# Performance work log

Measured on AMD Instinct MI355X. Metric: run time of the kernel, lower is better.

The kernel has to match this reference:

```python
import jax, jax.numpy as jnp
import numpy as np

B, S, D = 4, 2048, 512
H, DK, DV = 8, 64, 64


def setup_inputs() -> dict:
    key = jax.random.key(0)
    ks = jax.random.split(key, 9)
    inp = {
        "input_Q": jax.random.normal(ks[0], (B, S, D), dtype=jnp.float32),
        "input_K": jax.random.normal(ks[1], (B, S, D), dtype=jnp.float32),
        "input_V": jax.random.normal(ks[2], (B, S, D), dtype=jnp.float32),
        "attn_mask": jax.random.bernoulli(ks[3], 0.1, (B, S, S)),
        "other": jax.random.normal(ks[4], (B, S, S), dtype=jnp.float32),
        # nn.Linear weights stored [out_features, in_features]
        "W_Q": jax.random.normal(ks[5], (H * DK, D), dtype=jnp.float32) * (1.0 / np.sqrt(D)),
        "W_K": jax.random.normal(ks[6], (H * DK, D), dtype=jnp.float32) * (1.0 / np.sqrt(D)),
        "W_V": jax.random.normal(ks[7], (H * DV, D), dtype=jnp.float32) * (1.0 / np.sqrt(D)),
        "W_fc": jax.random.normal(ks[8], (D, H * DV), dtype=jnp.float32) * (1.0 / np.sqrt(H * DV)),
    }
    return inp


def reference(input_Q, input_K, input_V, attn_mask, other, W_Q, W_K, W_V, W_fc):
    b, s, _ = input_Q.shape
    # projections: y = x @ W.T, then split heads -> [B,H,S,dk]
    Q = (input_Q @ W_Q.T).reshape(b, s, H, DK).transpose(0, 2, 1, 3)
    K = (input_K @ W_K.T).reshape(b, s, H, DK).transpose(0, 2, 1, 3)
    V = (input_V @ W_V.T).reshape(b, s, H, DV).transpose(0, 2, 1, 3)
    scale = 1.0 / np.sqrt(DK).astype(np.float32)
    scores = jnp.einsum("bhqd,bhkd->bhqk", Q, K) * scale  # [B,H,S,S]
    scores = scores + other[:, None, :, :]  # additive bias broadcast over heads
    scores = jnp.where(attn_mask[:, None, :, :], jnp.float32(-1e9), scores)
    attn = jax.nn.softmax(scores, axis=-1)
    context = jnp.einsum("bhqk,bhkd->bhqd", attn, V)  # [B,H,S,DV]
    context = context.transpose(0, 2, 1, 3).reshape(b, s, H * DV)
    output = context @ W_fc.T  # dropout is identity at inference
    return (output, attn)
```

## Files before the change

### kernel.cpp

```cpp
#include <hip/hip_runtime.h>

#define BB 4
#define SS 2048
#define DDIM 512
#define HH 8
#define MTOK (BB*SS)
#define BHN (BB*HH)

typedef _Float16 f16;
typedef __attribute__((ext_vector_type(8))) _Float16 half8;
typedef __attribute__((ext_vector_type(4))) _Float16 half4;
typedef __attribute__((ext_vector_type(4))) float float4v;
typedef __attribute__((ext_vector_type(4))) int int4v;

#define SCALE_L2E 0.180336880073616f
#define L2E 1.44269504088896f
#define EBIAS 4.0f
#define MASKVAL -65504.0f

__device__ __forceinline__ float4v mfma_k32(half8 a, half8 b, float4v c) {
  return __builtin_amdgcn_mfma_f32_16x16x32_f16(a, b, c, 0, 0, 0);
}

__device__ __forceinline__ half8 cvt8(float4v a, float4v b) {
  half8 r;
  r[0] = (f16)a[0]; r[1] = (f16)a[1]; r[2] = (f16)a[2]; r[3] = (f16)a[3];
  r[4] = (f16)b[0]; r[5] = (f16)b[1]; r[6] = (f16)b[2]; r[7] = (f16)b[3];
  return r;
}

__global__ __launch_bounds__(256) void detect_mask_kernel(
    const unsigned int* __restrict__ m, unsigned int* __restrict__ flag) {
  unsigned int v = 0;
  const int base = blockIdx.x * 1024;
  for (int j = threadIdx.x; j < 1024; j += 256)
    if (m[base + j] > 1u) v = 1u;
  if (v) atomicOr(flag, 1u);
}

__global__ __launch_bounds__(256) void gemm_qkv(
    const float* __restrict__ inQ, const float* __restrict__ inK,
    const float* __restrict__ inV, const float* __restrict__ WQ,
    const float* __restrict__ WK, const float* __restrict__ WV,
    f16* __restrict__ Qp, f16* __restrict__ Kfrag, f16* __restrict__ Vfrag) {
  __shared__ f16 As[128][40];
  __shared__ f16 Bs[128][40];
  const int z = blockIdx.z;
  const float* A = (z == 0) ? inQ : (z == 1) ? inK : inV;
  const float* W = (z == 0) ? WQ : (z == 1) ? WK : WV;
  const int t = threadIdx.x;
  const int bm = blockIdx.x * 128;
  const int bn = blockIdx.y * 128;
  const int w = t >> 6, ln = t & 63;
  const int wr = w >> 1, wc = w & 1;
  const int lr = ln & 15, lg = ln >> 4;
  const int srow = t >> 1, scol = (t & 1) * 16;

  float4v acc[4][4] = {};

  for (int k0 = 0; k0 < 512; k0 += 32) {
    {
      const float* ap = A + (size_t)(bm + srow) * 512 + k0 + scol;
      float4v x0 = *(const float4v*)ap,       x1 = *(const float4v*)(ap + 4);
      float4v x2 = *(const float4v*)(ap + 8), x3 = *(const float4v*)(ap + 12);
      *(half8*)&As[srow][scol]     = cvt8(x0, x1);
      *(half8*)&As[srow][scol + 8] = cvt8(x2, x3);
    }
    {
      const float* wp = W + (size_t)(bn + srow) * 512 + k0 + scol;
      float4v x0 = *(const float4v*)wp,       x1 = *(const float4v*)(wp + 4);
      float4v x2 = *(const float4v*)(wp + 8), x3 = *(const float4v*)(wp + 12);
      *(half8*)&Bs[srow][scol]     = cvt8(x0, x1);
      *(half8*)&Bs[srow][scol + 8] = cvt8(x2, x3);
    }
    __syncthreads();
    half8 af[4], bf[4];
    #pragma unroll
    for (int m = 0; m < 4; m++) af[m] = *(const half8*)&As[wr * 64 + m * 16 + lr][lg * 8];
    #pragma unroll
    for (int n = 0; n < 4; n++) bf[n] = *(const half8*)&Bs[wc * 64 + n * 16 + lr][lg * 8];
    #pragma unroll
    for (int m = 0; m < 4; m++)
      #pragma unroll
      for (int n = 0; n < 4; n++) acc[m][n] = mfma_k32(af[m], bf[n], acc[m][n]);
    __syncthreads();
  }

  #pragma unroll
  for (int m = 0; m < 4; m++) {
    int row = bm + wr * 64 + m * 16 + lg * 4;
    #pragma unroll
    for (int n = 0; n < 4; n++) {
      int col = bn + wc * 64 + n * 16 + lr;
      int b_ = row >> 11, s_ = row & 2047, h_ = col >> 6, d_ = col & 63;
      if (z == 0) {
        #pragma unroll
        for (int r = 0; r < 4; r++)
          Qp[(size_t)(row + r) * 512 + col] = (f16)acc[m][n][r];
      } else if (z == 1) {
        #pragma unroll
        for (int r = 0; r < 4; r++) {
          int tok = s_ + r;
          Kfrag[((((size_t)(b_ * 8 + h_)) * 128 + (tok >> 4)) * 2 + (d_ >> 5)) * 512 +
                ((tok & 15) + 16 * ((d_ >> 3) & 3)) * 8 + (d_ & 7)] =
              (f16)acc[m][n][r];
        }
      } else {
        half4 ph;
        ph[0] = (f16)acc[m][n][0]; ph[1] = (f16)acc[m][n][1];
        ph[2] = (f16)acc[m][n][2]; ph[3] = (f16)acc[m][n][3];
        *(half4*)&Vfrag[((((size_t)(b_ * 8 + h_)) * 64 + (s_ >> 5)) * 4 + (d_ >> 4)) * 512 +
                        ((d_ & 15) + 16 * ((s_ >> 2) & 3)) * 8 + ((s_ >> 2) & 4)] = ph;
      }
    }
  }
}

__global__ __launch_bounds__(256) void gemm_out(const f16* __restrict__ ctx,
                                                const float* __restrict__ W,
                                                float* __restrict__ Out) {
  __shared__ f16 As[128][40];
  __shared__ f16 Bs[128][40];
  const int t = threadIdx.x;
  const int bm = blockIdx.x * 128;
  const int bn = blockIdx.y * 128;
  const int w = t >> 6, ln = t & 63;
  const int wr = w >> 1, wc = w & 1;
  const int lr = ln & 15, lg = ln >> 4;
  const int srow = t >> 1, scol = (t & 1) * 16;

  float4v acc[4][4] = {};

  for (int k0 = 0; k0 < 512; k0 += 32) {
    {
      const f16* ap = ctx + (size_t)(bm + srow) * 512 + k0 + scol;
      *(half8*)&As[srow][scol]     = *(const half8*)(ap);
      *(half8*)&As[srow][scol + 8] = *(const half8*)(ap + 8);
    }
    {
      const float* wp = W + (size_t)(bn + srow) * 512 + k0 + scol;
      float4v x0 = *(const float4v*)wp,       x1 = *(const float4v*)(wp + 4);
      float4v x2 = *(const float4v*)(wp + 8), x3 = *(const float4v*)(wp + 12);
      *(half8*)&Bs[srow][scol]     = cvt8(x0, x1);
      *(half8*)&Bs[srow][scol + 8] = cvt8(x2, x3);
    }
    __syncthreads();
    half8 af[4], bf[4];
    #pragma unroll
    for (int m = 0; m < 4; m++) af[m] = *(const half8*)&As[wr * 64 + m * 16 + lr][lg * 8];
    #pragma unroll
    for (int n = 0; n < 4; n++) bf[n] = *(const half8*)&Bs[wc * 64 + n * 16 + lr][lg * 8];
    #pragma unroll
    for (int m = 0; m < 4; m++)
      #pragma unroll
      for (int n = 0; n < 4; n++) acc[m][n] = mfma_k32(af[m], bf[n], acc[m][n]);
    __syncthreads();
  }

  #pragma unroll
  for (int m = 0; m < 4; m++) {
    int row = bm + wr * 64 + m * 16 + lg * 4;
    #pragma unroll
    for (int n = 0; n < 4; n++) {
      int col = bn + wc * 64 + n * 16 + lr;
      #pragma unroll
      for (int r = 0; r < 4; r++)
        Out[(size_t)(row + r) * 512 + col] = acc[m][n][r];
    }
  }
}

#define LOADT(dst, base, st) {                                  \
    const f16* p_ = (base) + (size_t)(st) * 2048;               \
    dst##0 = *(const half8*)(p_);                               \
    dst##1 = *(const half8*)(p_ + 512);                         \
    dst##2 = *(const half8*)(p_ + 1024);                        \
    dst##3 = *(const half8*)(p_ + 1536); }

__global__ __launch_bounds__(1024) void attn_fused(
    const f16* __restrict__ Qp, const f16* __restrict__ Kfrag,
    const f16* __restrict__ Vfrag, const float* __restrict__ other,
    const unsigned char* __restrict__ mask8, const int* __restrict__ mask32,
    const unsigned int* __restrict__ flag, float* __restrict__ attn_out,
    f16* __restrict__ ctx) {
  __shared__ f16 othm[16][2056];
  __shared__ float red[16][16];
  __shared__ float red2[16][16][66];

  const int t = threadIdx.x;
  const int bid = blockIdx.x;
  const int b = bid & 3;
  const int qblk = (bid >> 2) * 16;
  const int w = t >> 6, ln = t & 63;
  const int lr = ln & 15, lg = ln >> 4;
  const bool use8 = (*flag) != 0;

  {
    const int q = t >> 6, k0 = (t & 63) * 32;
    const size_t base = ((size_t)b * SS + qblk + q) * SS + k0;
    const float* op = other + base;
    if (use8) {
      const unsigned char* mp = mask8 + base;
      #pragma unroll
      for (int g = 0; g < 4; g++) {
        unsigned int mw0 = *(const unsigned int*)(mp + g * 8);
        unsigned int mw1 = *(const unsigned int*)(mp + g * 8 + 4);
        float4v o0 = *(const float4v*)(op + g * 8);
        float4v o1 = *(const float4v*)(op + g * 8 + 4);
        float4v r0, r1;
        #pragma unroll
        for (int r = 0; r < 4; r++) {
          r0[r] = ((mw0 >> (8 * r)) & 0xffu) ? MASKVAL : fmaf(o0[r], L2E, -EBIAS);
          r1[r] = ((mw1 >> (8 * r)) & 0xffu) ? MASKVAL : fmaf(o1[r], L2E, -EBIAS);
        }
        *(half8*)&othm[q][k0 + g * 8] = cvt8(r0, r1);
      }
    } else {
      const int* mp = mask32 + base;
      #pragma unroll
      for (int g = 0; g < 4; g++) {
        int4v m0 = *(const int4v*)(mp + g * 8);
        int4v m1 = *(const int4v*)(mp + g * 8 + 4);
        float4v o0 = *(const float4v*)(op + g * 8);
        float4v o1 = *(const float4v*)(op + g * 8 + 4);
        float4v r0, r1;
        #pragma unroll
        for (int r = 0; r < 4; r++) {
          r0[r] = m0[r] ? MASKVAL : fmaf(o0[r], L2E, -EBIAS);
          r1[r] = m1[r] ? MASKVAL : fmaf(o1[r], L2E, -EBIAS);
        }
        *(half8*)&othm[q][k0 + g * 8] = cvt8(r0, r1);
      }
    }
  }
  __syncthreads();

  const int q_g = qblk + lr;
  const f16* kfb = Kfrag + (size_t)(b * 8) * 131072 + ln * 8;
  const f16* vfb = Vfrag + (size_t)(b * 8) * 131072 + ln * 8;
  const f16* qpp = Qp + ((size_t)b * SS + q_g) * 512 + lg * 8;

  half8 qf0 = *(const half8*)(qpp);
  half8 qf1 = *(const half8*)(qpp + 32);

  half8 kA0, kA1, kA2, kA3, kB0, kB1, kB2, kB3;
  half8 vf0, vf1, vf2, vf3;

  LOADT(kA, kfb, w * 4 + 0);

  #define BODY(kf, edst, g) {                                             \
    float4v s0 = {}, s1 = {};                                             \
    s0 = mfma_k32(kf##0, qf0, s0);                                        \
    s0 = mfma_k32(kf##1, qf1, s0);                                        \
    s1 = mfma_k32(kf##2, qf0, s1);                                        \
    s1 = mfma_k32(kf##3, qf1, s1);                                        \
    const int kbase = w * 128 + (g) * 32;                                 \
    const half4 o40 = *(const half4*)&othm[lr][kbase + lg * 4];           \
    const half4 o41 = *(const half4*)&othm[lr][kbase + 16 + lg * 4];      \
    float4v ev0, ev1;                                                     \
    _Pragma("unroll")                                                     \
    for (int r = 0; r < 4; r++) {                                         \
      ev0[r] = exp2f(fmaf(s0[r], SCALE_L2E, (float)o40[r]));              \
      ev1[r] = exp2f(fmaf(s1[r], SCALE_L2E, (float)o41[r]));              \
    }                                                                     \
    rs += (ev0[0] + ev0[1]) + (ev0[2] + ev0[3]) +                         \
          (ev1[0] + ev1[1]) + (ev1[2] + ev1[3]);                          \
    edst = cvt8(ev0, ev1);                                                \
    cacc0 = mfma_k32(edst, vf0, cacc0);                                   \
    cacc1 = mfma_k32(edst, vf1, cacc1);                                   \
    cacc2 = mfma_k32(edst, vf2, cacc2);                                   \
    cacc3 = mfma_k32(edst, vf3, cacc3);                                   \
  }

  #define ASTORE(e, g) {                                                  \
    float4v av0, av1;                                                     \
    av0[0] = (float)e[0] * invl; av0[1] = (float)e[1] * invl;             \
    av0[2] = (float)e[2] * invl; av0[3] = (float)e[3] * invl;             \
    av1[0] = (float)e[4] * invl; av1[1] = (float)e[5] * invl;             \
    av1[2] = (float)e[6] * invl; av1[3] = (float)e[7] * invl;             \
    *(float4v*)(abase + (g) * 32 + lg * 4) = av0;                         \
    *(float4v*)(abase + (g) * 32 + 16 + lg * 4) = av1;                    \
  }

  for (int h = 0; h < 8; ++h) {
    const int bh = b * 8 + h;
    const f16* kfb_nx = (h < 7) ? kfb + 131072 : kfb;

    float rs = 0.f;
    float4v cacc0 = {}, cacc1 = {}, cacc2 = {}, cacc3 = {};
    half8 e0, e1, e2, e3;

    LOADT(vf, vfb, w * 4 + 0);
    LOADT(kB, kfb, w * 4 + 1);
    BODY(kA, e0, 0);

    LOADT(vf, vfb, w * 4 + 1);
    LOADT(kA, kfb, w * 4 + 2);
    BODY(kB, e1, 1);

    LOADT(vf, vfb, w * 4 + 2);
    LOADT(kB, kfb, w * 4 + 3);
    BODY(kA, e2, 2);

    LOADT(vf, vfb, w * 4 + 3);
    LOADT(kA, kfb_nx, w * 4 + 0);
    BODY(kB, e3, 3);

    const int hn = (h < 7) ? h + 1 : 7;
    half8 qn0 = *(const half8*)(qpp + hn * 64);
    half8 qn1 = *(const half8*)(qpp + hn * 64 + 32);

    rs += __shfl_xor(rs, 16);
    rs += __shfl_xor(rs, 32);
    if (ln < 16) red[w][lr] = rs;
    #pragma unroll
    for (int r = 0; r < 4; r++) {
      red2[w][lg * 4 + r][0 * 16 + lr] = cacc0[r];
      red2[w][lg * 4 + r][1 * 16 + lr] = cacc1[r];
      red2[w][lg * 4 + r][2 * 16 + lr] = cacc2[r];
      red2[w][lg * 4 + r][3 * 16 + lr] = cacc3[r];
    }
    __syncthreads();

    float lsum = 0.f;
    #pragma unroll
    for (int ww = 0; ww < 16; ww++) lsum += red[ww][lr];
    const float invl = 1.0f / lsum;

    float* abase = attn_out + ((size_t)bh * SS + q_g) * SS + w * 128;
    ASTORE(e0, 0);
    ASTORE(e1, 1);
    ASTORE(e2, 2);
    ASTORE(e3, 3);

    {
      float s16 = 0.f, l2 = 0.f;
      #pragma unroll
      for (int ww = 0; ww < 16; ww++) {
        s16 += red2[ww][w][ln];
        l2 += red[ww][w];
      }
      ctx[((size_t)b * SS + qblk + w) * 512 + h * 64 + ln] = (f16)(s16 / l2);
    }
    __syncthreads();

    qf0 = qn0;
    qf1 = qn1;
    kfb = kfb_nx;
    vfb = (h < 7) ? vfb + 131072 : vfb;
  }
  #undef BODY
  #undef ASTORE
}

extern "C" void kernel_launch(void* const* d_in, const int* in_sizes, int n_in,
                              void* d_out, int out_size, void* d_ws, size_t ws_size,
                              hipStream_t stream) {
  const float* inQ   = (const float*)d_in[0];
  const float* inK   = (const float*)d_in[1];
  const float* inV   = (const float*)d_in[2];
  const void*  mask  = d_in[3];
  const float* other = (const float*)d_in[4];
  const float* WQ    = (const float*)d_in[5];
  const float* WK    = (const float*)d_in[6];
  const float* WV    = (const float*)d_in[7];
  const float* WF    = (const float*)d_in[8];

  char* ws = (char*)d_ws;
  size_t off = 0;
  unsigned int* flag = (unsigned int*)(ws + off); off += 256;
  f16* Qp    = (f16*)(ws + off); off += (size_t)MTOK * 512 * 2;
  f16* Kfrag = (f16*)(ws + off); off += (size_t)MTOK * 512 * 2;
  f16* Vfrag = (f16*)(ws + off); off += (size_t)MTOK * 512 * 2;
  f16* ctx   = (f16*)(ws + off); off += (size_t)MTOK * 512 * 2;
  if (ws_size < off) return;

  float* outp  = (float*)d_out;
  float* attnp = outp + (size_t)MTOK * DDIM;

  hipMemsetAsync(flag, 0, 256, stream);
  detect_mask_kernel<<<64, 256, 0, stream>>>((const unsigned int*)mask, flag);

  gemm_qkv<<<dim3(64, 4, 3), 256, 0, stream>>>(inQ, inK, inV, WQ, WK, WV,
                                               Qp, Kfrag, Vfrag);

  attn_fused<<<512, 1024, 0, stream>>>(
      Qp, Kfrag, Vfrag, other, (const unsigned char*)mask, (const int*)mask,
      flag, attnp, ctx);

  gemm_out<<<dim3(64, 4), 256, 0, stream>>>(ctx, WF, outp);
}
```

Baseline: 334.1 us.

## Fuse output projection into attention kernel via LDS-resident context tile

```diff
diff --git a/kernel.cpp b/kernel.cpp
--- a/kernel.cpp
+++ b/kernel.cpp
@@ -116,60 +116,6 @@
   }
 }
 
-__global__ __launch_bounds__(256) void gemm_out(const f16* __restrict__ ctx,
-                                                const float* __restrict__ W,
-                                                float* __restrict__ Out) {
-  __shared__ f16 As[128][40];
-  __shared__ f16 Bs[128][40];
-  const int t = threadIdx.x;
-  const int bm = blockIdx.x * 128;
-  const int bn = blockIdx.y * 128;
-  const int w = t >> 6, ln = t & 63;
-  const int wr = w >> 1, wc = w & 1;
-  const int lr = ln & 15, lg = ln >> 4;
-  const int srow = t >> 1, scol = (t & 1) * 16;
-
-  float4v acc[4][4] = {};
-
-  for (int k0 = 0; k0 < 512; k0 += 32) {
-    {
-      const f16* ap = ctx + (size_t)(bm + srow) * 512 + k0 + scol;
-      *(half8*)&As[srow][scol]     = *(const half8*)(ap);
-      *(half8*)&As[srow][scol + 8] = *(const half8*)(ap + 8);
-    }
-    {
-      const float* wp = W + (size_t)(bn + srow) * 512 + k0 + scol;
-      float4v x0 = *(const float4v*)wp,       x1 = *(const float4v*)(wp + 4);
-      float4v x2 = *(const float4v*)(wp + 8), x3 = *(const float4v*)(wp + 12);
-      *(half8*)&Bs[srow][scol]     = cvt8(x0, x1);
-      *(half8*)&Bs[srow][scol + 8] = cvt8(x2, x3);
-    }
-    __syncthreads();
-    half8 af[4], bf[4];
-    #pragma unroll
-    for (int m = 0; m < 4; m++) af[m] = *(const half8*)&As[wr * 64 + m * 16 + lr][lg * 8];
-    #pragma unroll
-    for (int n = 0; n < 4; n++) bf[n] = *(const half8*)&Bs[wc * 64 + n * 16 + lr][lg * 8];
-    #pragma unroll
-    for (int m = 0; m < 4; m++)
-      #pragma unroll
-      for (int n = 0; n < 4; n++) acc[m][n] = mfma_k32(af[m], bf[n], acc[m][n]);
-    __syncthreads();
-  }
-
-  #pragma unroll
-  for (int m = 0; m < 4; m++) {
-    int row = bm + wr * 64 + m * 16 + lg * 4;
-    #pragma unroll
-    for (int n = 0; n < 4; n++) {
-      int col = bn + wc * 64 + n * 16 + lr;
-      #pragma unroll
-      for (int r = 0; r < 4; r++)
-        Out[(size_t)(row + r) * 512 + col] = acc[m][n][r];
-    }
-  }
-}
-
 #define LOADT(dst, base, st) {                                  \
     const f16* p_ = (base) + (size_t)(st) * 2048;               \
     dst##0 = *(const half8*)(p_);                               \
@@ -181,11 +127,12 @@
     const f16* __restrict__ Qp, const f16* __restrict__ Kfrag,
     const f16* __restrict__ Vfrag, const float* __restrict__ other,
     const unsigned char* __restrict__ mask8, const int* __restrict__ mask32,
-    const unsigned int* __restrict__ flag, float* __restrict__ attn_out,
-    f16* __restrict__ ctx) {
+    const unsigned int* __restrict__ flag, const float* __restrict__ WF,
+    float* __restrict__ attn_out, float* __restrict__ Out) {
   __shared__ f16 othm[16][2056];
   __shared__ float red[16][16];
   __shared__ float red2[16][16][66];
+  __shared__ f16 ctx_lds[16][520];
 
   const int t = threadIdx.x;
   const int bid = blockIdx.x;
@@ -326,23 +273,20 @@
     #pragma unroll
     for (int ww = 0; ww < 16; ww++) lsum += red[ww][lr];
     const float invl = 1.0f / lsum;
+    float s16 = 0.f, l2 = 0.f;
+    #pragma unroll
+    for (int ww = 0; ww < 16; ww++) {
+      s16 += red2[ww][w][ln];
+      l2 += red[ww][w];
+    }
+    __syncthreads();
 
     float* abase = attn_out + ((size_t)bh * SS + q_g) * SS + w * 128;
     ASTORE(e0, 0);
     ASTORE(e1, 1);
     ASTORE(e2, 2);
     ASTORE(e3, 3);
-
-    {
-      float s16 = 0.f, l2 = 0.f;
-      #pragma unroll
-      for (int ww = 0; ww < 16; ww++) {
-        s16 += red2[ww][w][ln];
-        l2 += red[ww][w];
-      }
-      ctx[((size_t)b * SS + qblk + w) * 512 + h * 64 + ln] = (f16)(s16 / l2);
-    }
-    __syncthreads();
+    ctx_lds[w][h * 64 + ln] = (f16)(s16 / l2);
 
     qf0 = qn0;
     qf1 = qn1;
@@ -351,6 +295,30 @@
   }
   #undef BODY
   #undef ASTORE
+
+  __syncthreads();
+
+  {
+    const float* wrow0 = WF + (size_t)(w * 32 + lr) * 512;
+    const float* wrow1 = WF + (size_t)(w * 32 + 16 + lr) * 512;
+    float4v oacc0 = {}, oacc1 = {};
+    #pragma unroll
+    for (int ks = 0; ks < 16; ks++) {
+      half8 af = *(const half8*)&ctx_lds[lr][ks * 32 + lg * 8];
+      float4v w00 = *(const float4v*)(wrow0 + ks * 32 + lg * 8);
+      float4v w01 = *(const float4v*)(wrow0 + ks * 32 + lg * 8 + 4);
+      float4v w10 = *(const float4v*)(wrow1 + ks * 32 + lg * 8);
+      float4v w11 = *(const float4v*)(wrow1 + ks * 32 + lg * 8 + 4);
+      oacc0 = mfma_k32(af, cvt8(w00, w01), oacc0);
+      oacc1 = mfma_k32(af, cvt8(w10, w11), oacc1);
+    }
+    #pragma unroll
+    for (int r = 0; r < 4; r++) {
+      float* ob = Out + ((size_t)b * SS + qblk + lg * 4 + r) * 512 + w * 32;
+      ob[lr] = oacc0[r];
+      ob[16 + lr] = oacc1[r];
+    }
+  }
 }
 
 extern "C" void kernel_launch(void* const* d_in, const int* in_sizes, int n_in,
@@ -372,7 +340,6 @@
   f16* Qp    = (f16*)(ws + off); off += (size_t)MTOK * 512 * 2;
   f16* Kfrag = (f16*)(ws + off); off += (size_t)MTOK * 512 * 2;
   f16* Vfrag = (f16*)(ws + off); off += (size_t)MTOK * 512 * 2;
-  f16* ctx   = (f16*)(ws + off); off += (size_t)MTOK * 512 * 2;
   if (ws_size < off) return;
 
   float* outp  = (float*)d_out;
@@ -386,7 +353,5 @@
 
   attn_fused<<<512, 1024, 0, stream>>>(
       Qp, Kfrag, Vfrag, other, (const unsigned char*)mask, (const int*)mask,
-      flag, attnp, ctx);
-
-  gemm_out<<<dim3(64, 4), 256, 0, stream>>>(ctx, WF, outp);
-}
+      flag, WF, attnp, outp);
+}
```

Result: slower. 403.9 us (+20.9%).
